# Kernel optimization log

Hardware: AMD Instinct MI355X
Metric: run time of the kernel (lower is better)

Reference implementation:

```python
import jax, jax.numpy as jnp
import numpy as np

EPS_LN = 1e-5
NEG_SLOPE = 0.2
NUM_GRAPHS = 64


def layer_norm(h, g, b):
    mu = h.mean(-1, keepdims=True)
    var = ((h - mu) ** 2).mean(-1, keepdims=True)
    return (h - mu) * jax.lax.rsqrt(var + EPS_LN) * g + b


def segment_softmax(alpha, dst, n):
    # alpha: [E2, H], softmax over edges sharing the same dst node
    m = jax.ops.segment_max(alpha, dst, num_segments=n)
    m = jnp.where(jnp.isfinite(m), m, 0.0)
    e = jnp.exp(alpha - m[dst])
    s = jax.ops.segment_sum(e, dst, num_segments=n)
    return e / (s[dst] + 1e-16)


def gat_conv(h, src, dst, eattr, W, We, a_s, a_d, a_e, bias, H, C):
    # PyG GATConv: shared src/dst linear, edge features, self-loops (fill='mean')
    N = h.shape[0]
    x = (h @ W).reshape(N, H, C)  # [N,H,C]
    loop = jnp.arange(N)
    src2 = jnp.concatenate([src, loop])
    dst2 = jnp.concatenate([dst, loop])
    loop_attr = jnp.broadcast_to(eattr.mean(0, keepdims=True), (N, eattr.shape[1]))
    e2 = jnp.concatenate([eattr, loop_attr], 0)
    eh = (e2 @ We).reshape(-1, H, C)  # [E2,H,C]
    alpha = (x * a_s).sum(-1)[src2] + (x * a_d).sum(-1)[dst2] + (eh * a_e).sum(-1)
    alpha = jax.nn.leaky_relu(alpha, NEG_SLOPE)  # [E2,H]
    alpha = segment_softmax(alpha, dst2, N)
    out = jax.ops.segment_sum(x[src2] * alpha[:, :, None], dst2, num_segments=N)
    return out.reshape(N, H * C) + bias


def setup_inputs():
    key = jax.random.key(0)
    ks = jax.random.split(key, 24)
    N, E = 50000, 400000
    Fin, Hd, H, ed = 6, 64, 4, 1
    d0 = Hd * H          # 256 after layer0
    C1 = 128 // H        # 32, layer1 per-head out
    s = 0.1
    inp = {
        'x': jax.random.normal(ks[0], (N, Fin), jnp.float32),
        'edge_index': jax.random.randint(ks[1], (2, E), 0, N),
        'edge_attr': jax.random.uniform(ks[2], (E, ed), jnp.float32),
        'batch': jnp.sort(jax.random.randint(ks[3], (N,), 0, NUM_GRAPHS)),
        'W_in': jax.random.normal(ks[4], (Fin, Hd), jnp.float32) * s,
        'b_in': jnp.zeros((Hd,), jnp.float32),
        'l0_W': jax.random.normal(ks[5], (Hd, H * Hd), jnp.float32) * s,
        'l0_We': jax.random.normal(ks[6], (ed, H * Hd), jnp.float32) * s,
        'l0_as': jax.random.normal(ks[7], (H, Hd), jnp.float32) * s,
        'l0_ad': jax.random.normal(ks[8], (H, Hd), jnp.float32) * s,
        'l0_ae': jax.random.normal(ks[9], (H, Hd), jnp.float32) * s,
        'l0_b': jnp.zeros((H * Hd,), jnp.float32),
        'ln0_g': jnp.ones((d0,), jnp.float32),
        'ln0_b': jnp.zeros((d0,), jnp.float32),
        'l1_W': jax.random.normal(ks[10], (d0, H * C1), jnp.float32) * s,
        'l1_We': jax.random.normal(ks[11], (ed, H * C1), jnp.float32) * s,
        'l1_as': jax.random.normal(ks[12], (H, C1), jnp.float32) * s,
        'l1_ad': jax.random.normal(ks[13], (H, C1), jnp.float32) * s,
        'l1_ae': jax.random.normal(ks[14], (H, C1), jnp.float32) * s,
        'l1_b': jnp.zeros((H * C1,), jnp.float32),
        'ln1_g': jnp.ones((128,), jnp.float32),
        'ln1_b': jnp.zeros((128,), jnp.float32),
    }
    return inp


def reference(x, edge_index, edge_attr, batch, W_in, b_in,
              l0_W, l0_We, l0_as, l0_ad, l0_ae, l0_b, ln0_g, ln0_b,
              l1_W, l1_We, l1_as, l1_ad, l1_ae, l1_b, ln1_g, ln1_b):
    src, dst = edge_index[0], edge_index[1]
    H = 4
    h = x @ W_in + b_in                                  # input_proj
    h = gat_conv(h, src, dst, edge_attr, l0_W, l0_We, l0_as, l0_ad, l0_ae, l0_b, H, 64)
    h = layer_norm(h, ln0_g, ln0_b)
    h = jax.nn.elu(h)                                    # dropout off (eval)
    h = gat_conv(h, src, dst, edge_attr, l1_W, l1_We, l1_as, l1_ad, l1_ae, l1_b, H, 32)
    h = layer_norm(h, ln1_g, ln1_b)
    cnt = jax.ops.segment_sum(jnp.ones((h.shape[0],), h.dtype), batch, num_segments=NUM_GRAPHS)
    h_mean = jax.ops.segment_sum(h, batch, num_segments=NUM_GRAPHS) / jnp.maximum(cnt, 1.0)[:, None]
    h_max = jax.ops.segment_max(h, batch, num_segments=NUM_GRAPHS)
    return (h_mean + h_max) / 2.0
```

## Files before the change

kernel.cpp:

```cpp
#include <hip/hip_runtime.h>
#include <math.h>

#define EPS_LN   1e-5f
#define NEG_SLOPE 0.2f
#define NUM_GRAPHS 64
#define POOL_SPLIT 16

__device__ __forceinline__ float red64(float v) {
    #pragma unroll
    for (int m = 32; m > 0; m >>= 1) v += __shfl_xor(v, m);
    return v;
}
__device__ __forceinline__ float red32(float v) {
    #pragma unroll
    for (int m = 16; m > 0; m >>= 1) v += __shfl_xor(v, m);
    return v;
}

__global__ __launch_bounds__(256) void k_input_proj(
    const float* __restrict__ x, const float* __restrict__ Win,
    const float* __restrict__ bin, float* __restrict__ h, int N)
{
    int t = blockIdx.x * 256 + threadIdx.x;
    if (t >= N * 64) return;
    int n = t >> 6, c = t & 63;
    float acc = bin[c];
    const float* xr = x + n * 6;
    #pragma unroll
    for (int k = 0; k < 6; ++k) acc += xr[k] * Win[k * 64 + c];
    h[t] = acc;
}

__global__ __launch_bounds__(256) void k_prep(
    const float* __restrict__ We0, const float* __restrict__ ae0,
    const float* __restrict__ We1, const float* __restrict__ ae1,
    float* __restrict__ wedot0, float* __restrict__ wedot1)
{
    __shared__ float red[256];
    int t = threadIdx.x;
    red[t] = We0[t] * ae0[t];
    __syncthreads();
    for (int s = 32; s > 0; s >>= 1) { if ((t & 63) < s) red[t] += red[t + s]; __syncthreads(); }
    if ((t & 63) == 0) wedot0[t >> 6] = red[t];
    __syncthreads();
    red[t] = (t < 128) ? We1[t] * ae1[t] : 0.f;
    __syncthreads();
    for (int s = 16; s > 0; s >>= 1) { if (t < 128 && (t & 31) < s) red[t] += red[t + s]; __syncthreads(); }
    if (t < 128 && (t & 31) == 0) wedot1[t >> 5] = red[t];
}

__global__ __launch_bounds__(256) void k_esum_partial(const float* __restrict__ ea, float* __restrict__ part, int E)
{
    __shared__ float red[256];
    int t = threadIdx.x;
    float s = 0.f;
    for (int i = blockIdx.x * 256 + t; i < E; i += gridDim.x * 256) s += ea[i];
    red[t] = s; __syncthreads();
    for (int k = 128; k > 0; k >>= 1) { if (t < k) red[t] += red[t + k]; __syncthreads(); }
    if (t == 0) part[blockIdx.x] = red[0];
}
__global__ __launch_bounds__(256) void k_esum_final(const float* __restrict__ part, int B, float* __restrict__ mean_out, int E)
{
    __shared__ float red[256];
    int t = threadIdx.x;
    red[t] = (t < B) ? part[t] : 0.f; __syncthreads();
    for (int k = 128; k > 0; k >>= 1) { if (t < k) red[t] += red[t + k]; __syncthreads(); }
    if (t == 0) *mean_out = red[0] / (float)E;
}

__global__ __launch_bounds__(256) void k_counts_init(int* __restrict__ counts, int N)
{
    int t = blockIdx.x * 256 + threadIdx.x;
    if (t < N) counts[t] = 1;
}
__global__ __launch_bounds__(256) void k_count(const int* __restrict__ dst, int* __restrict__ counts, int E)
{
    int e = blockIdx.x * 256 + threadIdx.x;
    if (e < E) atomicAdd(&counts[dst[e]], 1);
}
__global__ __launch_bounds__(256) void k_scan_partial(const int* __restrict__ counts, int* __restrict__ bsum, int N)
{
    __shared__ int red[256];
    int b = blockIdx.x, t = threadIdx.x;
    int base = b * 1024 + t * 4;
    int s = 0;
    #pragma unroll
    for (int i = 0; i < 4; ++i) { int idx = base + i; if (idx < N) s += counts[idx]; }
    red[t] = s; __syncthreads();
    for (int k = 128; k > 0; k >>= 1) { if (t < k) red[t] += red[t + k]; __syncthreads(); }
    if (t == 0) bsum[b] = red[0];
}
__global__ __launch_bounds__(64) void k_scan_bsums(const int* __restrict__ bsum, int* __restrict__ bpre, int B)
{
    __shared__ int s[64];
    int t = threadIdx.x;
    int v = (t < B) ? bsum[t] : 0;
    s[t] = v; __syncthreads();
    for (int off = 1; off < 64; off <<= 1) {
        int u = (t >= off) ? s[t - off] : 0; __syncthreads();
        s[t] += u; __syncthreads();
    }
    if (t < B) bpre[t] = s[t] - v;
}
__global__ __launch_bounds__(256) void k_scan_chunk(
    const int* __restrict__ counts, const int* __restrict__ bpre,
    int* __restrict__ row_ptr, int N, int E2)
{
    __shared__ int s[256];
    int b = blockIdx.x, t = threadIdx.x;
    int base = b * 1024 + t * 4;
    int l0 = (base + 0 < N) ? counts[base + 0] : 0;
    int l1 = (base + 1 < N) ? counts[base + 1] : 0;
    int l2 = (base + 2 < N) ? counts[base + 2] : 0;
    int l3 = (base + 3 < N) ? counts[base + 3] : 0;
    int lsum = l0 + l1 + l2 + l3;
    s[t] = lsum; __syncthreads();
    for (int off = 1; off < 256; off <<= 1) {
        int u = (t >= off) ? s[t - off] : 0; __syncthreads();
        s[t] += u; __syncthreads();
    }
    int run = bpre[b] + s[t] - lsum;
    if (base + 0 < N) row_ptr[base + 0] = run; run += l0;
    if (base + 1 < N) row_ptr[base + 1] = run; run += l1;
    if (base + 2 < N) row_ptr[base + 2] = run; run += l2;
    if (base + 3 < N) row_ptr[base + 3] = run;
    if (b == 0 && t == 0) row_ptr[N] = E2;
}
__global__ __launch_bounds__(256) void k_cursor_init(const int* __restrict__ row_ptr, int* __restrict__ cursor, int N)
{
    int t = blockIdx.x * 256 + threadIdx.x;
    if (t < N) cursor[t] = row_ptr[t];
}
__global__ __launch_bounds__(256) void k_place(
    const int* __restrict__ dst, int* __restrict__ cursor, int* __restrict__ eids, int E, int N)
{
    int e = blockIdx.x * 256 + threadIdx.x;
    if (e >= E + N) return;
    int d = (e < E) ? dst[e] : (e - E);
    int pos = atomicAdd(&cursor[d], 1);
    eids[pos] = e;
}
__global__ __launch_bounds__(256) void k_rowsort(const int* __restrict__ row_ptr, int* __restrict__ eids, int N)
{
    int n = blockIdx.x * 256 + threadIdx.x;
    if (n >= N) return;
    int r0 = row_ptr[n], r1 = row_ptr[n + 1];
    for (int i = r0 + 1; i < r1; ++i) {
        int key = eids[i];
        int j = i - 1;
        while (j >= r0 && eids[j] > key) { eids[j + 1] = eids[j]; --j; }
        eids[j + 1] = key;
    }
}

#define G0_NPW 4
__global__ __launch_bounds__(256) void k_gemm0(
    const float* __restrict__ h, const float* __restrict__ W0, float* __restrict__ x0, int N)
{
    __shared__ float Wl[64 * 256];
    int t = threadIdx.x;
    for (int i = t; i < 64 * 256; i += 256) Wl[i] = W0[i];
    __syncthreads();
    int wave = t >> 6, lane = t & 63;
    int gw = blockIdx.x * 4 + wave;
    int stride = gridDim.x * 4 * G0_NPW;
    for (int nb = gw * G0_NPW; nb < N; nb += stride) {
        float hv[G0_NPW];
        float acc[G0_NPW][4] = {};
        #pragma unroll
        for (int p = 0; p < G0_NPW; ++p) {
            int n = nb + p;
            hv[p] = (n < N) ? h[(size_t)n * 64 + lane] : 0.f;
        }
        for (int k = 0; k < 64; ++k) {
            float w0 = Wl[k * 256 + lane];
            float w1 = Wl[k * 256 + lane + 64];
            float w2 = Wl[k * 256 + lane + 128];
            float w3 = Wl[k * 256 + lane + 192];
            #pragma unroll
            for (int p = 0; p < G0_NPW; ++p) {
                float hk = __shfl(hv[p], k);
                acc[p][0] += hk * w0; acc[p][1] += hk * w1;
                acc[p][2] += hk * w2; acc[p][3] += hk * w3;
            }
        }
        #pragma unroll
        for (int p = 0; p < G0_NPW; ++p) {
            int n = nb + p;
            if (n < N) {
                float* o = x0 + (size_t)n * 256;
                o[lane] = acc[p][0]; o[lane + 64] = acc[p][1];
                o[lane + 128] = acc[p][2]; o[lane + 192] = acc[p][3];
            }
        }
    }
}

__global__ __launch_bounds__(256) void k_gemm1(
    const float* __restrict__ h0, const float* __restrict__ W1,
    float* __restrict__ x1, int N)
{
    __shared__ float Wc[32 * 128];
    __shared__ float Ht[32 * 128];
    const int nb = blockIdx.x * 128;
    const int t = threadIdx.x;
    const int tc = t & 15, tr = t >> 4;
    const int r0 = tr * 4, c0 = tc * 4;
    const int kg = t & 7, rb = t >> 3;
    float acc[8][8] = {};
    for (int kc = 0; kc < 8; ++kc) {
        __syncthreads();
        #pragma unroll
        for (int j = 0; j < 4; ++j) {
            int row = rb + j * 32;
            int n = nb + row;
            float4 v = make_float4(0.f, 0.f, 0.f, 0.f);
            if (n < N)
                v = *reinterpret_cast<const float4*>(h0 + (size_t)n * 256 + kc * 32 + kg * 4);
            #pragma unroll
            for (int i = 0; i < 4; ++i) {
                int k = kg * 4 + i;
                float e = (i == 0) ? v.x : (i == 1) ? v.y : (i == 2) ? v.z : v.w;
                Ht[k * 128 + (row ^ (k & 28))] = e;
            }
        }
        #pragma unroll
        for (int it = 0; it < 4; ++it) {
            int idx = t * 4 + it * 1024;
            int k2 = idx >> 7, c = idx & 127;
            *reinterpret_cast<float4*>(&Wc[idx]) =
                *reinterpret_cast<const float4*>(W1 + (size_t)(kc * 32 + k2) * 128 + c);
        }
        __syncthreads();
        #pragma unroll 4
        for (int k2 = 0; k2 < 32; ++k2) {
            int sw = k2 & 28;
            float4 hlo = *reinterpret_cast<const float4*>(&Ht[k2 * 128 + (r0 ^ sw)]);
            float4 hhi = *reinterpret_cast<const float4*>(&Ht[k2 * 128 + ((r0 + 64) ^ sw)]);
            float4 wlo = *reinterpret_cast<const float4*>(&Wc[k2 * 128 + c0]);
            float4 whi = *reinterpret_cast<const float4*>(&Wc[k2 * 128 + c0 + 64]);
            float hr[8] = {hlo.x, hlo.y, hlo.z, hlo.w, hhi.x, hhi.y, hhi.z, hhi.w};
            float wr[8] = {wlo.x, wlo.y, wlo.z, wlo.w, whi.x, whi.y, whi.z, whi.w};
            #pragma unroll
            for (int i = 0; i < 8; ++i)
                #pragma unroll
                for (int j = 0; j < 8; ++j)
                    acc[i][j] += hr[i] * wr[j];
        }
    }
    #pragma unroll
    for (int i = 0; i < 8; ++i) {
        int n = nb + ((i < 4) ? (r0 + i) : (r0 + 60 + i));
        if (n < N) {
            *reinterpret_cast<float4*>(x1 + (size_t)n * 128 + c0) =
                make_float4(acc[i][0], acc[i][1], acc[i][2], acc[i][3]);
            *reinterpret_cast<float4*>(x1 + (size_t)n * 128 + c0 + 64) =
                make_float4(acc[i][4], acc[i][5], acc[i][6], acc[i][7]);
        }
    }
}

template <int HC>
__global__ __launch_bounds__(256) void k_attn(
    const float* __restrict__ x, const float* __restrict__ a_s, const float* __restrict__ a_d,
    float* __restrict__ as_n, float* __restrict__ ad_n, int N)
{
    int n = (blockIdx.x * 256 + threadIdx.x) >> 6;
    int lane = threadIdx.x & 63;
    if (n >= N) return;
    const float* xr = x + (size_t)n * HC;
    #pragma unroll
    for (int j = 0; j < HC / 64; ++j) {
        int ch = j * 64 + lane;
        float v = xr[ch];
        float ps = v * a_s[ch], pd = v * a_d[ch];
        if (HC == 256) {
            ps = red64(ps); pd = red64(pd);
            if (lane == 0) { as_n[n * 4 + j] = ps; ad_n[n * 4 + j] = pd; }
        } else {
            ps = red32(ps); pd = red32(pd);
            if ((lane & 31) == 0) {
                int hh = 2 * j + (lane >> 5);
                as_n[n * 4 + hh] = ps; ad_n[n * 4 + hh] = pd;
            }
        }
    }
}

template <bool WRITE_SRC>
__global__ __launch_bounds__(256) void k_edgeprep(
    const int* __restrict__ row_ptr, const int* __restrict__ eids,
    const int* __restrict__ src, const float* __restrict__ eattr,
    const float* __restrict__ emean_p, const float* __restrict__ wedot,
    const float* __restrict__ as_n, const float* __restrict__ ad_n,
    int* __restrict__ srcp, float4* __restrict__ alpha, float* __restrict__ sinv,
    int N, int E)
{
    int n = (blockIdx.x * 256 + threadIdx.x) >> 6;
    int lane = threadIdx.x & 63;
    if (n >= N) return;
    float emean = *emean_p;
    float wd0 = wedot[0], wd1 = wedot[1], wd2 = wedot[2], wd3 = wedot[3];
    float adv0 = ad_n[n * 4 + 0], adv1 = ad_n[n * 4 + 1];
    float adv2 = ad_n[n * 4 + 2], adv3 = ad_n[n * 4 + 3];
    int r0 = row_ptr[n], r1 = row_ptr[n + 1];

    float m0 = -1e30f, m1 = -1e30f, m2 = -1e30f, m3 = -1e30f;
    for (int i = r0 + lane; i < r1; i += 64) {
        int eid = eids[i];
        int sn; float ev;
        if (eid < E) { sn = src[eid]; ev = eattr[eid]; } else { sn = n; ev = emean; }
        if (WRITE_SRC) srcp[i] = sn;
        const float* as4 = as_n + (size_t)sn * 4;
        float a0 = as4[0] + adv0 + ev * wd0;
        float a1 = as4[1] + adv1 + ev * wd1;
        float a2 = as4[2] + adv2 + ev * wd2;
        float a3 = as4[3] + adv3 + ev * wd3;
        a0 = (a0 > 0.f) ? a0 : NEG_SLOPE * a0;
        a1 = (a1 > 0.f) ? a1 : NEG_SLOPE * a1;
        a2 = (a2 > 0.f) ? a2 : NEG_SLOPE * a2;
        a3 = (a3 > 0.f) ? a3 : NEG_SLOPE * a3;
        m0 = fmaxf(m0, a0); m1 = fmaxf(m1, a1);
        m2 = fmaxf(m2, a2); m3 = fmaxf(m3, a3);
        alpha[i] = make_float4(a0, a1, a2, a3);
    }
    #pragma unroll
    for (int off = 32; off > 0; off >>= 1) {
        m0 = fmaxf(m0, __shfl_xor(m0, off));
        m1 = fmaxf(m1, __shfl_xor(m1, off));
        m2 = fmaxf(m2, __shfl_xor(m2, off));
        m3 = fmaxf(m3, __shfl_xor(m3, off));
    }
    float s0 = 0.f, s1 = 0.f, s2 = 0.f, s3 = 0.f;
    for (int i = r0 + lane; i < r1; i += 64) {
        float4 a = alpha[i];
        float w0 = __expf(a.x - m0), w1 = __expf(a.y - m1);
        float w2 = __expf(a.z - m2), w3 = __expf(a.w - m3);
        s0 += w0; s1 += w1; s2 += w2; s3 += w3;
        alpha[i] = make_float4(w0, w1, w2, w3);
    }
    #pragma unroll
    for (int off = 32; off > 0; off >>= 1) {
        s0 += __shfl_xor(s0, off); s1 += __shfl_xor(s1, off);
        s2 += __shfl_xor(s2, off); s3 += __shfl_xor(s3, off);
    }
    if (lane == 0) {
        sinv[n * 4 + 0] = 1.f / (s0 + 1e-16f);
        sinv[n * 4 + 1] = 1.f / (s1 + 1e-16f);
        sinv[n * 4 + 2] = 1.f / (s2 + 1e-16f);
        sinv[n * 4 + 3] = 1.f / (s3 + 1e-16f);
    }
}

template <int HC, int VEC, bool DO_ELU>
__global__ __launch_bounds__(256) void k_agg(
    const float* __restrict__ x, const int* __restrict__ row_ptr,
    const int* __restrict__ srcp, const float* __restrict__ alpha,
    const float* __restrict__ sinv,
    const float* __restrict__ bias, const float* __restrict__ lng, const float* __restrict__ lnb,
    float* __restrict__ out, int N)
{
    int n = (blockIdx.x * 256 + threadIdx.x) >> 6;
    int lane = threadIdx.x & 63;
    if (n >= N) return;
    int hh = lane >> 4;
    int r0 = row_ptr[n], r1 = row_ptr[n + 1];

    float acc[VEC] = {};
    for (int i = r0; i < r1; i += 8) {
        int cnt = min(r1 - i, 8);
        int sn[8]; float wv[8];
        #pragma unroll
        for (int j = 0; j < 8; ++j)
            if (j < cnt) { sn[j] = srcp[i + j]; wv[j] = alpha[(size_t)(i + j) * 4 + hh]; }
        #pragma unroll
        for (int j = 0; j < 8; ++j)
            if (j < cnt) {
                const float* xr = x + (size_t)sn[j] * HC + lane * VEC;
                if constexpr (VEC == 4) {
                    float4 xv = *reinterpret_cast<const float4*>(xr);
                    acc[0] += wv[j] * xv.x; acc[1] += wv[j] * xv.y;
                    acc[2] += wv[j] * xv.z; acc[3] += wv[j] * xv.w;
                } else {
                    float2 xv = *reinterpret_cast<const float2*>(xr);
                    acc[0] += wv[j] * xv.x; acc[1] += wv[j] * xv.y;
                }
            }
    }
    float inv = sinv[n * 4 + hh];

    int ch0 = lane * VEC;
    float v[VEC];
    #pragma unroll
    for (int i = 0; i < VEC; ++i) v[i] = acc[i] * inv + bias[ch0 + i];
    float ls = 0.f;
    #pragma unroll
    for (int i = 0; i < VEC; ++i) ls += v[i];
    ls = red64(ls);
    float mu = ls / (float)HC;
    float lv = 0.f;
    #pragma unroll
    for (int i = 0; i < VEC; ++i) { float d = v[i] - mu; lv += d * d; }
    lv = red64(lv);
    float rs = rsqrtf(lv / (float)HC + EPS_LN);
    float o[VEC];
    #pragma unroll
    for (int i = 0; i < VEC; ++i) {
        float y = (v[i] - mu) * rs * lng[ch0 + i] + lnb[ch0 + i];
        if (DO_ELU) y = (y > 0.f) ? y : (expm1f(y));
        o[i] = y;
    }
    float* orow = out + (size_t)n * HC + ch0;
    if constexpr (VEC == 4) *reinterpret_cast<float4*>(orow) = make_float4(o[0], o[1], o[2], o[3]);
    else                    *reinterpret_cast<float2*>(orow) = make_float2(o[0], o[1]);
}

__global__ __launch_bounds__(128) void k_bounds(const int* __restrict__ batch, int* __restrict__ gstart, int N)
{
    int g = threadIdx.x;
    if (g > NUM_GRAPHS) return;
    int lo = 0, hi = N;
    while (lo < hi) { int mid = (lo + hi) >> 1; if (batch[mid] < g) lo = mid + 1; else hi = mid; }
    gstart[g] = lo;
}
__global__ __launch_bounds__(128) void k_pool1(
    const float* __restrict__ h1, const int* __restrict__ gstart,
    float* __restrict__ psum, float* __restrict__ pmax)
{
    int g = blockIdx.x, sl = blockIdx.y, c = threadIdx.x;
    int s0 = gstart[g], s1 = gstart[g + 1];
    int cnt = s1 - s0;
    int chunk = (cnt + POOL_SPLIT - 1) / POOL_SPLIT;
    int b0 = s0 + sl * chunk;
    int b1 = min(b0 + chunk, s1);
    float sum = 0.f, mx = -INFINITY;
    for (int n = b0; n < b1; ++n) {
        float v = h1[(size_t)n * 128 + c];
        sum += v; mx = fmaxf(mx, v);
    }
    int o = (g * POOL_SPLIT + sl) * 128 + c;
    psum[o] = sum; pmax[o] = mx;
}
__global__ __launch_bounds__(128) void k_pool2(
    const float* __restrict__ psum, const float* __restrict__ pmax,
    const int* __restrict__ gstart, float* __restrict__ out)
{
    int g = blockIdx.x, c = threadIdx.x;
    float sum = 0.f, mx = -INFINITY;
    #pragma unroll
    for (int sl = 0; sl < POOL_SPLIT; ++sl) {
        int o = (g * POOL_SPLIT + sl) * 128 + c;
        sum += psum[o];
        mx = fmaxf(mx, pmax[o]);
    }
    int cnt = gstart[g + 1] - gstart[g];
    float mean = sum / fmaxf((float)cnt, 1.f);
    out[g * 128 + c] = 0.5f * (mean + mx);
}

extern "C" void kernel_launch(void* const* d_in, const int* in_sizes, int n_in,
                              void* d_out, int out_size, void* d_ws, size_t ws_size,
                              hipStream_t stream)
{
    const float* x     = (const float*)d_in[0];
    const int*   ei    = (const int*)d_in[1];
    const float* eattr = (const float*)d_in[2];
    const int*   batch = (const int*)d_in[3];
    const float* Win   = (const float*)d_in[4];
    const float* bin   = (const float*)d_in[5];
    const float* l0W   = (const float*)d_in[6];
    const float* l0We  = (const float*)d_in[7];
    const float* l0as  = (const float*)d_in[8];
    const float* l0ad  = (const float*)d_in[9];
    const float* l0ae  = (const float*)d_in[10];
    const float* l0b   = (const float*)d_in[11];
    const float* ln0g  = (const float*)d_in[12];
    const float* ln0b  = (const float*)d_in[13];
    const float* l1W   = (const float*)d_in[14];
    const float* l1We  = (const float*)d_in[15];
    const float* l1as  = (const float*)d_in[16];
    const float* l1ad  = (const float*)d_in[17];
    const float* l1ae  = (const float*)d_in[18];
    const float* l1b   = (const float*)d_in[19];
    const float* ln1g  = (const float*)d_in[20];
    const float* ln1b  = (const float*)d_in[21];

    const int N = in_sizes[0] / 6;
    const int E = in_sizes[1] / 2;
    const int E2 = E + N;
    const int* srcI = ei;
    const int* dstI = ei + E;

    char* ws = (char*)d_ws;
    size_t off = 0;
    auto alloc = [&](size_t bytes) -> char* {
        char* p = ws + off;
        off += (bytes + 255) & ~(size_t)255;
        return p;
    };

    float* h      = (float*)alloc((size_t)N * 64 * 4);
    float* x0     = (float*)alloc((size_t)N * 256 * 4);
    float* h0     = (float*)alloc((size_t)N * 256 * 4);
    float* as0    = (float*)alloc((size_t)N * 4 * 4);
    float* ad0    = (float*)alloc((size_t)N * 4 * 4);
    float* as1    = (float*)alloc((size_t)N * 4 * 4);
    float* ad1    = (float*)alloc((size_t)N * 4 * 4);
    float* sinv   = (float*)alloc((size_t)N * 4 * 4);
    int*   row_ptr= (int*)alloc((size_t)(N + 1) * 4);
    int*   counts = (int*)alloc((size_t)N * 4);
    int*   cursor = (int*)alloc((size_t)N * 4);
    int*   eids   = (int*)alloc((size_t)E2 * 4);
    int*   srcp   = (int*)alloc((size_t)E2 * 4);
    float4* alphab= (float4*)alloc((size_t)E2 * 16);
    int*   bsum   = (int*)alloc(64 * 4);
    int*   bpre   = (int*)alloc(64 * 4);
    float* epart  = (float*)alloc(256 * 4);
    float* emean  = (float*)alloc(4);
    float* wedot0 = (float*)alloc(16);
    float* wedot1 = (float*)alloc(16);
    int*   gstart = (int*)alloc((NUM_GRAPHS + 1) * 4);
    float* psum   = (float*)alloc((size_t)NUM_GRAPHS * POOL_SPLIT * 128 * 4);
    float* pmax   = (float*)alloc((size_t)NUM_GRAPHS * POOL_SPLIT * 128 * 4);

    float* x1 = x0;
    float* h1 = x0 + (size_t)N * 128;

    const int B = (N + 1023) / 1024;

    k_input_proj<<<(N * 64 + 255) / 256, 256, 0, stream>>>(x, Win, bin, h, N);
    k_prep<<<1, 256, 0, stream>>>(l0We, l0ae, l1We, l1ae, wedot0, wedot1);
    k_esum_partial<<<256, 256, 0, stream>>>(eattr, epart, E);
    k_esum_final<<<1, 256, 0, stream>>>(epart, 256, emean, E);

    k_counts_init<<<(N + 255) / 256, 256, 0, stream>>>(counts, N);
    k_count<<<(E + 255) / 256, 256, 0, stream>>>(dstI, counts, E);
    k_scan_partial<<<B, 256, 0, stream>>>(counts, bsum, N);
    k_scan_bsums<<<1, 64, 0, stream>>>(bsum, bpre, B);
    k_scan_chunk<<<B, 256, 0, stream>>>(counts, bpre, row_ptr, N, E2);
    k_cursor_init<<<(N + 255) / 256, 256, 0, stream>>>(row_ptr, cursor, N);
    k_place<<<(E2 + 255) / 256, 256, 0, stream>>>(dstI, cursor, eids, E, N);
    k_rowsort<<<(N + 255) / 256, 256, 0, stream>>>(row_ptr, eids, N);

    k_gemm0<<<512, 256, 0, stream>>>(h, l0W, x0, N);
    k_attn<256><<<(N + 3) / 4, 256, 0, stream>>>(x0, l0as, l0ad, as0, ad0, N);
    k_edgeprep<true><<<(N + 3) / 4, 256, 0, stream>>>(
        row_ptr, eids, srcI, eattr, emean, wedot0, as0, ad0, srcp, alphab, sinv, N, E);
    k_agg<256, 4, true><<<(N + 3) / 4, 256, 0, stream>>>(
        x0, row_ptr, srcp, (const float*)alphab, sinv, l0b, ln0g, ln0b, h0, N);

    k_gemm1<<<(N + 127) / 128, 256, 0, stream>>>(h0, l1W, x1, N);
    k_attn<128><<<(N + 3) / 4, 256, 0, stream>>>(x1, l1as, l1ad, as1, ad1, N);
    k_edgeprep<false><<<(N + 3) / 4, 256, 0, stream>>>(
        row_ptr, eids, srcI, eattr, emean, wedot1, as1, ad1, srcp, alphab, sinv, N, E);
    k_agg<128, 2, false><<<(N + 3) / 4, 256, 0, stream>>>(
        x1, row_ptr, srcp, (const float*)alphab, sinv, l1b, ln1g, ln1b, h1, N);

    k_bounds<<<1, 128, 0, stream>>>(batch, gstart, N);
    k_pool1<<<dim3(NUM_GRAPHS, POOL_SPLIT), 128, 0, stream>>>(h1, gstart, psum, pmax);
    k_pool2<<<NUM_GRAPHS, 128, 0, stream>>>(psum, pmax, gstart, (float*)d_out);
}
```

Measured before the change: 457.4 us.

## Fuse attention-score dot products into GEMM epilogues and cursor init into scan

The per-node source and destination attention dot products are now computed in the epilogues of both linear-projection GEMM kernels, using warp shuffles on the accumulators already in registers. This removes the two separate k_attn kernels, which re-read the full projected feature matrices from memory. The cursor initialisation is also folded into the scan kernel, dropping one more launch. In exchange the GEMM epilogues carry extra shuffle reductions and register pressure, and k_gemm1's per-head reduction depends on the thread-to-column mapping being exact.

```diff
diff --git a/kernel.cpp b/kernel.cpp
--- a/kernel.cpp
+++ b/kernel.cpp
@@ -9,11 +9,6 @@
 __device__ __forceinline__ float red64(float v) {
     #pragma unroll
     for (int m = 32; m > 0; m >>= 1) v += __shfl_xor(v, m);
-    return v;
-}
-__device__ __forceinline__ float red32(float v) {
-    #pragma unroll
-    for (int m = 16; m > 0; m >>= 1) v += __shfl_xor(v, m);
     return v;
 }
 
@@ -104,7 +99,7 @@
 }
 __global__ __launch_bounds__(256) void k_scan_chunk(
     const int* __restrict__ counts, const int* __restrict__ bpre,
-    int* __restrict__ row_ptr, int N, int E2)
+    int* __restrict__ row_ptr, int* __restrict__ cursor, int N, int E2)
 {
     __shared__ int s[256];
     int b = blockIdx.x, t = threadIdx.x;
@@ -120,16 +115,11 @@
         s[t] += u; __syncthreads();
     }
     int run = bpre[b] + s[t] - lsum;
-    if (base + 0 < N) row_ptr[base + 0] = run; run += l0;
-    if (base + 1 < N) row_ptr[base + 1] = run; run += l1;
-    if (base + 2 < N) row_ptr[base + 2] = run; run += l2;
-    if (base + 3 < N) row_ptr[base + 3] = run;
+    if (base + 0 < N) { row_ptr[base + 0] = run; cursor[base + 0] = run; } run += l0;
+    if (base + 1 < N) { row_ptr[base + 1] = run; cursor[base + 1] = run; } run += l1;
+    if (base + 2 < N) { row_ptr[base + 2] = run; cursor[base + 2] = run; } run += l2;
+    if (base + 3 < N) { row_ptr[base + 3] = run; cursor[base + 3] = run; }
     if (b == 0 && t == 0) row_ptr[N] = E2;
-}
-__global__ __launch_bounds__(256) void k_cursor_init(const int* __restrict__ row_ptr, int* __restrict__ cursor, int N)
-{
-    int t = blockIdx.x * 256 + threadIdx.x;
-    if (t < N) cursor[t] = row_ptr[t];
 }
 __global__ __launch_bounds__(256) void k_place(
     const int* __restrict__ dst, int* __restrict__ cursor, int* __restrict__ eids, int E, int N)
@@ -155,13 +145,18 @@
 
 #define G0_NPW 4
 __global__ __launch_bounds__(256) void k_gemm0(
-    const float* __restrict__ h, const float* __restrict__ W0, float* __restrict__ x0, int N)
+    const float* __restrict__ h, const float* __restrict__ W0,
+    const float* __restrict__ As, const float* __restrict__ Ad,
+    float* __restrict__ x0, float* __restrict__ as0, float* __restrict__ ad0, int N)
 {
     __shared__ float Wl[64 * 256];
     int t = threadIdx.x;
     for (int i = t; i < 64 * 256; i += 256) Wl[i] = W0[i];
     __syncthreads();
     int wave = t >> 6, lane = t & 63;
+    float asv[4], adv[4];
+    #pragma unroll
+    for (int j = 0; j < 4; ++j) { asv[j] = As[j * 64 + lane]; adv[j] = Ad[j * 64 + lane]; }
     int gw = blockIdx.x * 4 + wave;
     int stride = gridDim.x * 4 * G0_NPW;
     for (int nb = gw * G0_NPW; nb < N; nb += stride) {
@@ -192,13 +187,20 @@
                 o[lane] = acc[p][0]; o[lane + 64] = acc[p][1];
                 o[lane + 128] = acc[p][2]; o[lane + 192] = acc[p][3];
             }
+            #pragma unroll
+            for (int j = 0; j < 4; ++j) {
+                float ps = red64(acc[p][j] * asv[j]);
+                float pd = red64(acc[p][j] * adv[j]);
+                if (lane == 0 && n < N) { as0[n * 4 + j] = ps; ad0[n * 4 + j] = pd; }
+            }
         }
     }
 }
 
 __global__ __launch_bounds__(256) void k_gemm1(
     const float* __restrict__ h0, const float* __restrict__ W1,
-    float* __restrict__ x1, int N)
+    const float* __restrict__ As, const float* __restrict__ Ad,
+    float* __restrict__ x1, float* __restrict__ as1, float* __restrict__ ad1, int N)
 {
     __shared__ float Wc[32 * 128];
     __shared__ float Ht[32 * 128];
@@ -207,6 +209,12 @@
     const int tc = t & 15, tr = t >> 4;
     const int r0 = tr * 4, c0 = tc * 4;
     const int kg = t & 7, rb = t >> 3;
+    float asv[8], adv[8];
+    #pragma unroll
+    for (int j = 0; j < 8; ++j) {
+        int col = c0 + ((j < 4) ? j : 60 + j);
+        asv[j] = As[col]; adv[j] = Ad[col];
+    }
     float acc[8][8] = {};
     for (int kc = 0; kc < 8; ++kc) {
         __syncthreads();
@@ -257,32 +265,19 @@
             *reinterpret_cast<float4*>(x1 + (size_t)n * 128 + c0 + 64) =
                 make_float4(acc[i][4], acc[i][5], acc[i][6], acc[i][7]);
         }
-    }
-}
-
-template <int HC>
-__global__ __launch_bounds__(256) void k_attn(
-    const float* __restrict__ x, const float* __restrict__ a_s, const float* __restrict__ a_d,
-    float* __restrict__ as_n, float* __restrict__ ad_n, int N)
-{
-    int n = (blockIdx.x * 256 + threadIdx.x) >> 6;
-    int lane = threadIdx.x & 63;
-    if (n >= N) return;
-    const float* xr = x + (size_t)n * HC;
-    #pragma unroll
-    for (int j = 0; j < HC / 64; ++j) {
-        int ch = j * 64 + lane;
-        float v = xr[ch];
-        float ps = v * a_s[ch], pd = v * a_d[ch];
-        if (HC == 256) {
-            ps = red64(ps); pd = red64(pd);
-            if (lane == 0) { as_n[n * 4 + j] = ps; ad_n[n * 4 + j] = pd; }
-        } else {
-            ps = red32(ps); pd = red32(pd);
-            if ((lane & 31) == 0) {
-                int hh = 2 * j + (lane >> 5);
-                as_n[n * 4 + hh] = ps; ad_n[n * 4 + hh] = pd;
-            }
+        float sA = acc[i][0] * asv[0] + acc[i][1] * asv[1] + acc[i][2] * asv[2] + acc[i][3] * asv[3];
+        float sB = acc[i][4] * asv[4] + acc[i][5] * asv[5] + acc[i][6] * asv[6] + acc[i][7] * asv[7];
+        float dA = acc[i][0] * adv[0] + acc[i][1] * adv[1] + acc[i][2] * adv[2] + acc[i][3] * adv[3];
+        float dB = acc[i][4] * adv[4] + acc[i][5] * adv[5] + acc[i][6] * adv[6] + acc[i][7] * adv[7];
+        #pragma unroll
+        for (int off = 1; off <= 4; off <<= 1) {
+            sA += __shfl_xor(sA, off); sB += __shfl_xor(sB, off);
+            dA += __shfl_xor(dA, off); dB += __shfl_xor(dB, off);
+        }
+        if ((tc & 7) == 0 && n < N) {
+            int hA = tc >> 3;
+            as1[n * 4 + hA] = sA; as1[n * 4 + 2 + hA] = sB;
+            ad1[n * 4 + hA] = dA; ad1[n * 4 + 2 + hA] = dB;
         }
     }
 }
@@ -537,20 +532,17 @@
     k_count<<<(E + 255) / 256, 256, 0, stream>>>(dstI, counts, E);
     k_scan_partial<<<B, 256, 0, stream>>>(counts, bsum, N);
     k_scan_bsums<<<1, 64, 0, stream>>>(bsum, bpre, B);
-    k_scan_chunk<<<B, 256, 0, stream>>>(counts, bpre, row_ptr, N, E2);
-    k_cursor_init<<<(N + 255) / 256, 256, 0, stream>>>(row_ptr, cursor, N);
+    k_scan_chunk<<<B, 256, 0, stream>>>(counts, bpre, row_ptr, cursor, N, E2);
     k_place<<<(E2 + 255) / 256, 256, 0, stream>>>(dstI, cursor, eids, E, N);
     k_rowsort<<<(N + 255) / 256, 256, 0, stream>>>(row_ptr, eids, N);
 
-    k_gemm0<<<512, 256, 0, stream>>>(h, l0W, x0, N);
-    k_attn<256><<<(N + 3) / 4, 256, 0, stream>>>(x0, l0as, l0ad, as0, ad0, N);
+    k_gemm0<<<512, 256, 0, stream>>>(h, l0W, l0as, l0ad, x0, as0, ad0, N);
     k_edgeprep<true><<<(N + 3) / 4, 256, 0, stream>>>(
         row_ptr, eids, srcI, eattr, emean, wedot0, as0, ad0, srcp, alphab, sinv, N, E);
     k_agg<256, 4, true><<<(N + 3) / 4, 256, 0, stream>>>(
         x0, row_ptr, srcp, (const float*)alphab, sinv, l0b, ln0g, ln0b, h0, N);
 
-    k_gemm1<<<(N + 127) / 128, 256, 0, stream>>>(h0, l1W, x1, N);
-    k_attn<128><<<(N + 3) / 4, 256, 0, stream>>>(x1, l1as, l1ad, as1, ad1, N);
+    k_gemm1<<<(N + 127) / 128, 256, 0, stream>>>(h0, l1W, l1as, l1ad, x1, as1, ad1, N);
     k_edgeprep<false><<<(N + 3) / 4, 256, 0, stream>>>(
         row_ptr, eids, srcI, eattr, emean, wedot1, as1, ad1, srcp, alphab, sinv, N, E);
     k_agg<128, 2, false><<<(N + 3) / 4, 256, 0, stream>>>(
```

Result: faster. 442.8 us (-3.2%).
